# Performance work log

Measured on AMD Instinct MI355X. Metric: run time of the kernel, lower is better.

The kernel has to match this reference:

```python
import jax, jax.numpy as jnp
import numpy as np

D_IN = 1024
D_OUT = 1024
N = 4096


def setup_inputs() -> dict:
    key = jax.random.key(0)
    ks = jax.random.split(key, 7)
    s_in = 1.0 / np.sqrt(D_IN)
    return {
        "x": jax.random.normal(ks[0], (N, D_IN), dtype=jnp.float32),
        "W_q": jax.random.uniform(ks[1], (D_IN, D_OUT), jnp.float32, -s_in, s_in),
        "b_q": jax.random.uniform(ks[2], (D_OUT,), jnp.float32, -s_in, s_in),
        "W_k": jax.random.uniform(ks[3], (D_IN, D_OUT), jnp.float32, -s_in, s_in),
        "b_k": jax.random.uniform(ks[4], (D_OUT,), jnp.float32, -s_in, s_in),
        "W_v": jax.random.uniform(ks[5], (D_IN, D_OUT), jnp.float32, -s_in, s_in),
        "b_v": jax.random.uniform(ks[6], (D_OUT,), jnp.float32, -s_in, s_in),
    }


def reference(x, W_q, b_q, W_k, b_k, W_v, b_v):
    # QKV projections (Linear with bias): [N, d_out]
    q = x @ W_q + b_q
    k = x @ W_k + b_k
    v = x @ W_v + b_v
    # Full attention: scores [N, N], scaled by sqrt(d_out)
    scores = (q @ k.T) / jnp.sqrt(jnp.asarray(k.shape[-1], q.dtype))
    attn = jax.nn.softmax(scores, axis=-1)
    return attn @ v  # [N, d_out]
```

## Files before the change

### kernel.cpp

```cpp
#include <hip/hip_runtime.h>

typedef __attribute__((ext_vector_type(8))) short short8;
typedef __attribute__((ext_vector_type(4))) float f32x4;
typedef __attribute__((ext_vector_type(8))) unsigned short ushort8;

typedef const unsigned int __attribute__((address_space(1)))* gas1_t;
typedef unsigned int __attribute__((address_space(3)))* las3_t;

__device__ __forceinline__ void gload_lds16(const void* g, void* l) {
  __builtin_amdgcn_global_load_lds((gas1_t)g, (las3_t)l, 16, 0, 0);
}

__device__ __forceinline__ unsigned short f2bf(float f) {
  unsigned int u = __float_as_uint(f);
  u += 0x7FFFu + ((u >> 16) & 1u);
  return (unsigned short)(u >> 16);
}
__device__ __forceinline__ float bf2f(unsigned short b) {
  return __uint_as_float(((unsigned int)b) << 16);
}

__global__ __launch_bounds__(256) void conv_f32_bf16(const float* __restrict__ in,
                                                     unsigned short* __restrict__ out, int n8) {
  int i = blockIdx.x * 256 + threadIdx.x;
  if (i >= n8) return;
  const f32x4* p = (const f32x4*)(in + (size_t)i * 8);
  f32x4 a = p[0], b = p[1];
  ushort8 o;
  o[0]=f2bf(a[0]); o[1]=f2bf(a[1]); o[2]=f2bf(a[2]); o[3]=f2bf(a[3]);
  o[4]=f2bf(b[0]); o[5]=f2bf(b[1]); o[6]=f2bf(b[2]); o[7]=f2bf(b[3]);
  *(ushort8*)(out + (size_t)i * 8) = o;
}

__global__ __launch_bounds__(256) void transconv_w(const float* __restrict__ Wq,
                                                   const float* __restrict__ Wk,
                                                   const float* __restrict__ Wv,
                                                   unsigned short* __restrict__ out) {
  __shared__ unsigned short tile[64][66];
  const float* W = (blockIdx.z == 0) ? Wq : ((blockIdx.z == 1) ? Wk : Wv);
  unsigned short* O = out + (size_t)blockIdx.z * 1048576;
  const int bi = blockIdx.x * 64;
  const int bo = blockIdx.y * 64;
#pragma unroll
  for (int p = 0; p < 16; ++p) {
    int idx = p * 256 + threadIdx.x;
    int r = idx >> 6, c = idx & 63;
    tile[r][c] = f2bf(W[(size_t)(bi + r) * 1024 + bo + c]);
  }
  __syncthreads();
#pragma unroll
  for (int p = 0; p < 16; ++p) {
    int idx = p * 256 + threadIdx.x;
    int r = idx >> 6, c = idx & 63;
    O[(size_t)(bo + r) * 1024 + bi + c] = tile[c][r];
  }
}

__global__ __launch_bounds__(256) void trans_bf16(const unsigned short* __restrict__ in,
                                                  unsigned short* __restrict__ out, int R, int C) {
  __shared__ unsigned short tile[64][66];
  const int br = blockIdx.x * 64, bc = blockIdx.y * 64;
#pragma unroll
  for (int p = 0; p < 16; ++p) {
    int idx = p * 256 + threadIdx.x;
    int r = idx >> 6, c = idx & 63;
    tile[r][c] = in[(size_t)(br + r) * C + bc + c];
  }
  __syncthreads();
#pragma unroll
  for (int p = 0; p < 16; ++p) {
    int idx = p * 256 + threadIdx.x;
    int r = idx >> 6, c = idx & 63;
    out[(size_t)(bc + r) * R + br + c] = tile[c][r];
  }
}

__global__ __launch_bounds__(256) void reduce_pv(const unsigned short* __restrict__ P,
                                                 const float* __restrict__ rsum,
                                                 float* __restrict__ out) {
  int i = blockIdx.x * 256 + threadIdx.x;
  const int m = (i * 8) >> 10;
  const float inv = 1.0f / rsum[m];
  float s[8] = {0.f, 0.f, 0.f, 0.f, 0.f, 0.f, 0.f, 0.f};
#pragma unroll
  for (int z = 0; z < 4; ++z) {
    ushort8 v = *(const ushort8*)(P + (size_t)z * 4194304 + (size_t)i * 8);
#pragma unroll
    for (int j = 0; j < 8; ++j) s[j] += bf2f(v[j]);
  }
  f32x4 o0, o1;
#pragma unroll
  for (int j = 0; j < 4; ++j) { o0[j] = s[j] * inv; o1[j] = s[4 + j] * inv; }
  f32x4* po = (f32x4*)(out + (size_t)i * 8);
  po[0] = o0; po[1] = o1;
}

template <int EPI>
__global__ __launch_bounds__(512, 1) void gemm256(
    const unsigned short* __restrict__ A, const unsigned short* __restrict__ B,
    int lda, int ldb, int K, void* __restrict__ C, int ldc,
    size_t strideBz, size_t strideCz,
    const float* __restrict__ bq, const float* __restrict__ bk, const float* __restrict__ bv,
    float scale, float* __restrict__ rsum) {
  __shared__ unsigned short As[2][2][8192];
  __shared__ unsigned short Bs[2][2][8192];
  const int tid = threadIdx.x;
  const int lane = tid & 63;
  const int w = tid >> 6;
  const int wr = w >> 2;
  const int wc = w & 3;
  const int l16 = lane & 15;
  const int q = lane >> 4;

  const int nwgx = gridDim.x;
  const int nwg = nwgx * gridDim.y;
  const int lin = blockIdx.y * nwgx + blockIdx.x;
  const int swz = (lin & 7) * (nwg >> 3) + (lin >> 3);
  const int m0 = (swz / nwgx) * 256;
  const int n0 = (swz % nwgx) * 256;
  const int z = blockIdx.z;
  const unsigned short* Bz = B + (size_t)z * strideBz;
  const size_t koff = (EPI == 2) ? (size_t)z * K : 0;

  f32x4 acc[8][4];
#pragma unroll
  for (int i = 0; i < 8; ++i)
#pragma unroll
    for (int j = 0; j < 4; ++j) acc[i][j] = f32x4{0.f, 0.f, 0.f, 0.f};

  const unsigned short* ap[2][2];
  const unsigned short* bp[2][2];
#pragma unroll
  for (int h = 0; h < 2; ++h)
#pragma unroll
    for (int j = 0; j < 2; ++j) {
      const int g = (j << 9) + tid;
      const int row = g >> 3;
      const int cb = (g & 7) ^ (row & 7);
      ap[h][j] = A + (size_t)(m0 + h * 128 + row) * lda + koff + cb * 8;
      bp[h][j] = Bz + (size_t)(n0 + h * 128 + row) * ldb + koff + cb * 8;
    }

#define STG(buf, k0)                                                          \
  do {                                                                        \
    _Pragma("unroll") for (int _h = 0; _h < 2; ++_h) {                        \
      _Pragma("unroll") for (int _j = 0; _j < 2; ++_j) {                      \
        gload_lds16(ap[_h][_j] + (k0), &As[buf][_h][((_j << 9) + tid) * 8]);  \
        gload_lds16(bp[_h][_j] + (k0), &Bs[buf][_h][((_j << 9) + tid) * 8]);  \
      }                                                                       \
    }                                                                         \
  } while (0)

  const int NT = K / 64;
  STG(0, 0);
  STG(1, 64);

  for (int t = 0; t < NT; ++t) {
    const int cur = t & 1;
    if (t + 1 < NT) {
      asm volatile("s_waitcnt vmcnt(8)" ::: "memory");
    } else {
      asm volatile("s_waitcnt vmcnt(0)" ::: "memory");
    }
    __builtin_amdgcn_sched_barrier(0);
    __builtin_amdgcn_s_barrier();
    __builtin_amdgcn_sched_barrier(0);

#pragma unroll
    for (int ks = 0; ks < 2; ++ks) {
      const int sw = ((ks << 2) + q) ^ (l16 & 7);
      short8 bfr[4], afr[8];
#pragma unroll
      for (int ni = 0; ni < 4; ++ni) {
        const int r = ((wc & 1) << 6) + ni * 16 + l16;
        bfr[ni] = *(const short8*)(&Bs[cur][wc >> 1][r * 64 + sw * 8]);
      }
#pragma unroll
      for (int mi = 0; mi < 8; ++mi) {
        const int r = mi * 16 + l16;
        afr[mi] = *(const short8*)(&As[cur][wr][r * 64 + sw * 8]);
      }
#pragma unroll
      for (int mi = 0; mi < 8; ++mi)
#pragma unroll
        for (int ni = 0; ni < 4; ++ni)
          acc[mi][ni] = __builtin_amdgcn_mfma_f32_16x16x32_bf16(afr[mi], bfr[ni], acc[mi][ni], 0, 0, 0);
    }

    __builtin_amdgcn_sched_barrier(0);
    __builtin_amdgcn_s_barrier();
    __builtin_amdgcn_sched_barrier(0);
    if (t + 2 < NT) STG(cur, (t + 2) * 64);
  }
#undef STG

  const int row0 = m0 + wr * 128 + q * 4;
  const int col0 = n0 + wc * 64;

  if constexpr (EPI == 0) {
    unsigned short* O = (unsigned short*)C + (size_t)z * strideCz;
    const float* bias = (z == 0) ? bq : ((z == 1) ? bk : bv);
#pragma unroll
    for (int mi = 0; mi < 8; ++mi)
#pragma unroll
      for (int ni = 0; ni < 4; ++ni) {
        const int col = col0 + ni * 16 + l16;
        const int row = row0 + mi * 16;
        float bvv = bias[col];
#pragma unroll
        for (int r = 0; r < 4; ++r)
          O[(size_t)(row + r) * ldc + col] = f2bf(acc[mi][ni][r] + bvv);
      }
  } else if constexpr (EPI == 1) {
    unsigned short* O = (unsigned short*)C;
#pragma unroll
    for (int mi = 0; mi < 8; ++mi) {
      float rs[4] = {0.f, 0.f, 0.f, 0.f};
      const int row = row0 + mi * 16;
#pragma unroll
      for (int ni = 0; ni < 4; ++ni) {
        const int col = col0 + ni * 16 + l16;
#pragma unroll
        for (int r = 0; r < 4; ++r) {
          unsigned short ub = f2bf(__expf(acc[mi][ni][r] * scale));
          O[(size_t)(row + r) * ldc + col] = ub;
          rs[r] += bf2f(ub);
        }
      }
#pragma unroll
      for (int off = 1; off <= 8; off <<= 1) {
#pragma unroll
        for (int r = 0; r < 4; ++r) rs[r] += __shfl_xor(rs[r], off);
      }
      if (l16 == 0) {
#pragma unroll
        for (int r = 0; r < 4; ++r) unsafeAtomicAdd(&rsum[row + r], rs[r]);
      }
    }
  } else {
    unsigned short* O = (unsigned short*)C + (size_t)z * strideCz;
#pragma unroll
    for (int mi = 0; mi < 8; ++mi)
#pragma unroll
      for (int ni = 0; ni < 4; ++ni) {
        const int col = col0 + ni * 16 + l16;
        const int row = row0 + mi * 16;
#pragma unroll
        for (int r = 0; r < 4; ++r)
          O[(size_t)(row + r) * ldc + col] = f2bf(acc[mi][ni][r]);
      }
  }
}

extern "C" void kernel_launch(void* const* d_in, const int* in_sizes, int n_in,
                              void* d_out, int out_size, void* d_ws, size_t ws_size,
                              hipStream_t stream) {
  const float* x  = (const float*)d_in[0];
  const float* Wq = (const float*)d_in[1];
  const float* bq = (const float*)d_in[2];
  const float* Wk = (const float*)d_in[3];
  const float* bk = (const float*)d_in[4];
  const float* Wv = (const float*)d_in[5];
  const float* bv = (const float*)d_in[6];
  float* out = (float*)d_out;
  char* ws = (char*)d_ws;
  const size_t MB = 1024 * 1024;

  unsigned short* xb  = (unsigned short*)(ws + 0);
  unsigned short* wt  = (unsigned short*)(ws + 8 * MB);
  unsigned short* qkv = (unsigned short*)(ws + 14 * MB);
  unsigned short* qb  = qkv;
  unsigned short* kb  = qkv + (size_t)4194304;
  unsigned short* vb  = qkv + (size_t)2 * 4194304;
  float*          rsum= (float*)(ws + 37 * MB);
  unsigned short* vt  = (unsigned short*)(ws + 38 * MB);
  unsigned short* S   = (unsigned short*)(ws + 46 * MB);
  unsigned short* P   = (unsigned short*)(ws + 0);

  conv_f32_bf16<<<2048, 256, 0, stream>>>(x, xb, 524288);
  transconv_w<<<dim3(16, 16, 3), 256, 0, stream>>>(Wq, Wk, Wv, wt);
  gemm256<0><<<dim3(4, 16, 3), 512, 0, stream>>>(
      xb, wt, 1024, 1024, 1024, qkv, 1024,
      (size_t)1048576, (size_t)4194304, bq, bk, bv, 1.0f, nullptr);
  trans_bf16<<<dim3(64, 16), 256, 0, stream>>>(vb, vt, 4096, 1024);
  hipMemsetAsync(rsum, 0, 4096 * sizeof(float), stream);
  gemm256<1><<<dim3(16, 16), 512, 0, stream>>>(
      qb, kb, 1024, 1024, 1024, S, 4096,
      (size_t)0, (size_t)0, nullptr, nullptr, nullptr, 0.03125f, rsum);
  gemm256<2><<<dim3(4, 16, 4), 512, 0, stream>>>(
      S, vt, 4096, 4096, 1024, P, 1024,
      (size_t)0, (size_t)4194304, nullptr, nullptr, nullptr, 1.0f, nullptr);
  reduce_pv<<<2048, 256, 0, stream>>>(P, rsum, out);
}
```

Measured before the change: 156.0 us.

## Restructure GEMM main loop into fine-grained 8-phase ping-pong pipeline

Changes the LDS layout from 64-wide k rows split by M/N halves to 32-wide k-slices with a new XOR swizzle. The main loop is unrolled by two k-tiles and split into eight phases, each interleaving partial LDS fragment loads and per-slice global-to-LDS staging with a 4x4 MFMA block. s_setprio raises priority around the MFMAs. The aim is to overlap global loads, LDS reads and matrix math more finely and to cut register pressure for fragments. The cost is many more barriers per tile, and the loop now assumes an even number of k-tiles.

After: 148.8 us. 4.6% less time.

```diff
diff --git a/kernel.cpp b/kernel.cpp
--- a/kernel.cpp
+++ b/kernel.cpp
@@ -111,6 +111,7 @@
   const int wc = w & 3;
   const int l16 = lane & 15;
   const int q = lane >> 4;
+  const int swq = (q ^ ((l16 >> 1) & 3)) * 8;
 
   const int nwgx = gridDim.x;
   const int nwg = nwgx * gridDim.y;
@@ -128,71 +129,115 @@
 #pragma unroll
     for (int j = 0; j < 4; ++j) acc[i][j] = f32x4{0.f, 0.f, 0.f, 0.f};
 
-  const unsigned short* ap[2][2];
-  const unsigned short* bp[2][2];
-#pragma unroll
-  for (int h = 0; h < 2; ++h)
+  const unsigned short* apA[2][2];
+  const unsigned short* apB[2][2];
+#pragma unroll
+  for (int ks = 0; ks < 2; ++ks)
 #pragma unroll
     for (int j = 0; j < 2; ++j) {
       const int g = (j << 9) + tid;
-      const int row = g >> 3;
-      const int cb = (g & 7) ^ (row & 7);
-      ap[h][j] = A + (size_t)(m0 + h * 128 + row) * lda + koff + cb * 8;
-      bp[h][j] = Bz + (size_t)(n0 + h * 128 + row) * ldb + koff + cb * 8;
+      const int row = g >> 2;
+      const int sq = (g & 3) ^ ((row >> 1) & 3);
+      apA[ks][j] = A + (size_t)(m0 + row) * lda + koff + ks * 32 + sq * 8;
+      apB[ks][j] = Bz + (size_t)(n0 + row) * ldb + koff + ks * 32 + sq * 8;
     }
 
-#define STG(buf, k0)                                                          \
-  do {                                                                        \
-    _Pragma("unroll") for (int _h = 0; _h < 2; ++_h) {                        \
-      _Pragma("unroll") for (int _j = 0; _j < 2; ++_j) {                      \
-        gload_lds16(ap[_h][_j] + (k0), &As[buf][_h][((_j << 9) + tid) * 8]);  \
-        gload_lds16(bp[_h][_j] + (k0), &Bs[buf][_h][((_j << 9) + tid) * 8]);  \
-      }                                                                       \
+#define STG_A(BUF, KS, K0)                                      \
+  do {                                                          \
+    gload_lds16(apA[KS][0] + (K0), &As[BUF][KS][tid * 8]);      \
+    gload_lds16(apA[KS][1] + (K0), &As[BUF][KS][(512 + tid) * 8]); \
+  } while (0)
+#define STG_B(BUF, KS, K0)                                      \
+  do {                                                          \
+    gload_lds16(apB[KS][0] + (K0), &Bs[BUF][KS][tid * 8]);      \
+    gload_lds16(apB[KS][1] + (K0), &Bs[BUF][KS][(512 + tid) * 8]); \
+  } while (0)
+
+  short8 bfr[4], afr[4];
+#define LDB4(KS, BUF)                                                         \
+  do {                                                                        \
+    _Pragma("unroll") for (int _n = 0; _n < 4; ++_n) {                        \
+      const int _r = wc * 64 + _n * 16 + l16;                                 \
+      bfr[_n] = *(const short8*)(&Bs[BUF][KS][_r * 32 + swq]);                \
     }                                                                         \
   } while (0)
+#define LDA4(KS, MH, BUF)                                                     \
+  do {                                                                        \
+    _Pragma("unroll") for (int _m = 0; _m < 4; ++_m) {                        \
+      const int _r = wr * 128 + ((MH) * 4 + _m) * 16 + l16;                   \
+      afr[_m] = *(const short8*)(&As[BUF][KS][_r * 32 + swq]);                \
+    }                                                                         \
+  } while (0)
+#define MMP(MH)                                                               \
+  do {                                                                        \
+    __builtin_amdgcn_s_setprio(1);                                            \
+    _Pragma("unroll") for (int _m = 0; _m < 4; ++_m)                          \
+      _Pragma("unroll") for (int _n = 0; _n < 4; ++_n)                        \
+        acc[(MH) * 4 + _m][_n] = __builtin_amdgcn_mfma_f32_16x16x32_bf16(     \
+            afr[_m], bfr[_n], acc[(MH) * 4 + _m][_n], 0, 0, 0);               \
+    __builtin_amdgcn_s_setprio(0);                                            \
+  } while (0)
+#define PH_SYNC                                                               \
+  do {                                                                        \
+    __builtin_amdgcn_sched_barrier(0);                                        \
+    __builtin_amdgcn_s_barrier();                                             \
+    asm volatile("s_waitcnt lgkmcnt(0)" ::: "memory");                        \
+    __builtin_amdgcn_sched_barrier(0);                                        \
+  } while (0)
+#define PH_END                                                                \
+  do {                                                                        \
+    __builtin_amdgcn_sched_barrier(0);                                        \
+    __builtin_amdgcn_s_barrier();                                             \
+    __builtin_amdgcn_sched_barrier(0);                                        \
+  } while (0)
 
   const int NT = K / 64;
-  STG(0, 0);
-  STG(1, 64);
-
-  for (int t = 0; t < NT; ++t) {
-    const int cur = t & 1;
-    if (t + 1 < NT) {
-      asm volatile("s_waitcnt vmcnt(8)" ::: "memory");
-    } else {
-      asm volatile("s_waitcnt vmcnt(0)" ::: "memory");
+  STG_B(0, 0, 0); STG_A(0, 0, 0); STG_B(0, 1, 0); STG_A(0, 1, 0);
+  if (1 < NT) { STG_B(1, 0, 64); STG_A(1, 0, 64); STG_B(1, 1, 64); }
+  if (1 < NT) asm volatile("s_waitcnt vmcnt(6)" ::: "memory");
+  else        asm volatile("s_waitcnt vmcnt(0)" ::: "memory");
+  __builtin_amdgcn_s_barrier();
+
+  for (int t = 0; t < NT; t += 2) {
+    const bool more = (t + 2 < NT);
+    const int k2 = (t + 2) * 64, k3 = (t + 3) * 64;
+    LDB4(0, 0); LDA4(0, 0, 0);
+    STG_A(1, 1, (t + 1) * 64);
+    PH_SYNC; MMP(0); PH_END;
+    LDA4(0, 1, 0);
+    if (more) STG_B(0, 0, k2);
+    PH_SYNC; MMP(1); PH_END;
+    LDB4(1, 0); LDA4(1, 0, 0);
+    if (more) STG_A(0, 0, k2);
+    PH_SYNC; MMP(0); PH_END;
+    LDA4(1, 1, 0);
+    if (more) STG_B(0, 1, k2);
+    if (more) asm volatile("s_waitcnt vmcnt(6)" ::: "memory");
+    else      asm volatile("s_waitcnt vmcnt(0)" ::: "memory");
+    PH_SYNC; MMP(1); PH_END;
+    LDB4(0, 1); LDA4(0, 0, 1);
+    if (more) STG_A(0, 1, k2);
+    PH_SYNC; MMP(0); PH_END;
+    LDA4(0, 1, 1);
+    if (more) STG_B(1, 0, k3);
+    PH_SYNC; MMP(1); PH_END;
+    LDB4(1, 1); LDA4(1, 0, 1);
+    if (more) STG_A(1, 0, k3);
+    PH_SYNC; MMP(0); PH_END;
+    LDA4(1, 1, 1);
+    if (more) {
+      STG_B(1, 1, k3);
+      asm volatile("s_waitcnt vmcnt(6)" ::: "memory");
     }
-    __builtin_amdgcn_sched_barrier(0);
-    __builtin_amdgcn_s_barrier();
-    __builtin_amdgcn_sched_barrier(0);
-
-#pragma unroll
-    for (int ks = 0; ks < 2; ++ks) {
-      const int sw = ((ks << 2) + q) ^ (l16 & 7);
-      short8 bfr[4], afr[8];
-#pragma unroll
-      for (int ni = 0; ni < 4; ++ni) {
-        const int r = ((wc & 1) << 6) + ni * 16 + l16;
-        bfr[ni] = *(const short8*)(&Bs[cur][wc >> 1][r * 64 + sw * 8]);
-      }
-#pragma unroll
-      for (int mi = 0; mi < 8; ++mi) {
-        const int r = mi * 16 + l16;
-        afr[mi] = *(const short8*)(&As[cur][wr][r * 64 + sw * 8]);
-      }
-#pragma unroll
-      for (int mi = 0; mi < 8; ++mi)
-#pragma unroll
-        for (int ni = 0; ni < 4; ++ni)
-          acc[mi][ni] = __builtin_amdgcn_mfma_f32_16x16x32_bf16(afr[mi], bfr[ni], acc[mi][ni], 0, 0, 0);
-    }
-
-    __builtin_amdgcn_sched_barrier(0);
-    __builtin_amdgcn_s_barrier();
-    __builtin_amdgcn_sched_barrier(0);
-    if (t + 2 < NT) STG(cur, (t + 2) * 64);
-  }
-#undef STG
+    PH_SYNC; MMP(1); PH_END;
+  }
+#undef STG_A
+#undef STG_B
+#undef LDB4
+#undef LDA4
+#undef MMP
+#undef PH_SYNC
+#undef PH_END
 
   const int row0 = m0 + wr * 128 + q * 4;
   const int col0 = n0 + wc * 64;
```
